# Optimization experiments

Measured on AMD Instinct MI355X. Metric: run time of the kernel, lower is better.

## Reference

```python
import jax, jax.numpy as jnp
import numpy as np
import math

B, N, DIM, H, DH, NNULL = 2, 2048, 1024, 16, 64, 2
SCALE = 8.0
LN_EPS = 1e-5


def _alibi_slopes(heads):
    # heads is a power of 2 here (16): slopes = start * start**i
    start = 2.0 ** (-(2.0 ** (-(math.log2(heads) - 3))))
    return np.array([start * (start ** i) for i in range(heads)], dtype=np.float32)


def setup_inputs() -> dict:
    key = jax.random.key(0)
    ks = jax.random.split(key, 6)
    inner = H * DH
    return {
        "x": jax.random.normal(ks[0], (B, N, DIM), dtype=jnp.float32),
        "norm_g": jnp.ones((DIM,), jnp.float32),
        "norm_b": jnp.zeros((DIM,), jnp.float32),
        "Wq": jax.random.normal(ks[1], (DIM, inner), jnp.float32) * 0.02,
        "Wkv": jax.random.normal(ks[2], (DIM, 2 * inner), jnp.float32) * 0.02,
        "q_scale": jnp.ones((DH,), jnp.float32),
        "k_scale": jnp.ones((DH,), jnp.float32),
        "null_kv": jax.random.normal(ks[3], (H, 2 * NNULL, DH), jnp.float32),
        "Wout": jax.random.normal(ks[4], (inner, DIM), jnp.float32) * 0.02,
    }


def _l2norm(t):
    # matches F.normalize: x / max(||x||, 1e-12)
    n = jnp.sqrt(jnp.sum(t * t, axis=-1, keepdims=True))
    return t / jnp.maximum(n, 1e-12)


def reference(x, norm_g, norm_b, Wq, Wkv, q_scale, k_scale, null_kv, Wout):
    b, n, dim = x.shape
    h, dh, nn = H, DH, NNULL
    j = n + nn

    # NOTE: faithful to source -- K/V come from the PRE-norm x (kv_input bound
    # before x = self.norm(x)); only Q uses the LayerNorm'd x.
    mu = jnp.mean(x, axis=-1, keepdims=True)
    var = jnp.mean((x - mu) ** 2, axis=-1, keepdims=True)
    xn = (x - mu) * jax.lax.rsqrt(var + LN_EPS) * norm_g + norm_b

    q = (xn @ Wq).reshape(b, n, h, dh).transpose(0, 2, 1, 3)          # b h n d
    kv = x @ Wkv
    k, v = jnp.split(kv, 2, axis=-1)
    k = k.reshape(b, n, h, dh).transpose(0, 2, 1, 3)                   # b h n d
    v = v.reshape(b, n, h, dh).transpose(0, 2, 1, 3)

    # null kv: (h, 2*nn, dh) -> (h, nn, 2, dh)
    null = null_kv.reshape(h, nn, 2, dh)
    nk = jnp.broadcast_to(null[:, :, 0, :][None], (b, h, nn, dh))
    nv = jnp.broadcast_to(null[:, :, 1, :][None], (b, h, nn, dh))
    k = jnp.concatenate([nk, k], axis=2)                               # b h j d
    v = jnp.concatenate([nv, v], axis=2)

    q = _l2norm(q) * q_scale
    k = _l2norm(k) * k_scale

    sim = jnp.einsum('bhid,bhjd->bhij', q, k) * SCALE                  # b h n j

    # ALiBi bias: rows at positions j-n..j-1, cols 0..j-1
    irow = jnp.arange(j - n, j)
    jcol = jnp.arange(j)
    bias = -jnp.abs(jcol[None, :] - irow[:, None]).astype(sim.dtype)   # (n, j)
    slopes = jnp.asarray(_alibi_slopes(h))[:, None, None]              # (h,1,1)
    sim = sim + slopes * bias

    # causal mask: triu with offset j - n + 1 (null kv always visible)
    causal = jnp.triu(jnp.ones((n, j), dtype=bool), k=j - n + 1)
    neg = jnp.finfo(sim.dtype).max
    sim = jnp.where(causal[None, None], -neg, sim)

    attn = jax.nn.softmax(sim, axis=-1)
    out = jnp.einsum('bhij,bhjd->bhid', attn, v)
    out = out.transpose(0, 2, 1, 3).reshape(b, n, h * dh)
    return out @ Wout
```

## Files before the change

### kernel.cpp

```cpp
#include <hip/hip_runtime.h>
#include <hip/hip_bf16.h>
#include <stdint.h>

#define H_    16
#define N_    2048
#define DIM_  1024
#define DH_   64
#define NN_   2
#define J_    2050
#define JP_   2112
#define B_    2
#define M_    4096
#define NSEG_ 84

typedef unsigned short u16;
typedef unsigned int u32;
typedef short bf16x8 __attribute__((ext_vector_type(8)));
typedef float f32x4 __attribute__((ext_vector_type(4)));

__device__ __forceinline__ u16 f2b(float f) {
  union { float f; unsigned int i; } v; v.f = f;
  unsigned int r = v.i + 0x7fffu + ((v.i >> 16) & 1u);
  return (u16)(r >> 16);
}
__device__ __forceinline__ float b2f(u16 u) {
  union { unsigned int i; float f; } v; v.i = ((unsigned int)u) << 16; return v.f;
}
__device__ __forceinline__ float lo2f(u32 u) {
  union { u32 i; float f; } v; v.i = u << 16; return v.f;
}
__device__ __forceinline__ float hi2f(u32 u) {
  union { u32 i; float f; } v; v.i = u & 0xffff0000u; return v.f;
}
__device__ __forceinline__ void unp8(const uint4 u, float* d) {
  d[0] = lo2f(u.x); d[1] = hi2f(u.x); d[2] = lo2f(u.y); d[3] = hi2f(u.y);
  d[4] = lo2f(u.z); d[5] = hi2f(u.z); d[6] = lo2f(u.w); d[7] = hi2f(u.w);
}
__device__ __forceinline__ u32 pk2(float a, float b) {
  union { __hip_bfloat162 h; u32 u; } x;
  x.h = __float22bfloat162_rn(make_float2(a, b));
  return x.u;
}
__device__ __forceinline__ void dma16(const u16* g, u16* l) {
  __builtin_amdgcn_global_load_lds(
      (const __attribute__((address_space(1))) u32*)(const void*)g,
      (__attribute__((address_space(3))) u32*)(void*)l, 16, 0, 0);
}

__global__ __launch_bounds__(256) void wtrans_k(const float* __restrict__ Wq,
                                                const float* __restrict__ Wkv,
                                                const float* __restrict__ Wout,
                                                u16* __restrict__ WqT,
                                                u16* __restrict__ WkvT,
                                                u16* __restrict__ WoutT) {
  __shared__ float tile[32][33];
  int bx = blockIdx.x;
  const float* in; u16* out; int C, cx;
  if (bx < 32)      { in = Wq;   out = WqT;   C = 1024; cx = bx; }
  else if (bx < 96) { in = Wkv;  out = WkvT;  C = 2048; cx = bx - 32; }
  else              { in = Wout; out = WoutT; C = 1024; cx = bx - 96; }
  const int R = 1024;
  int tx = threadIdx.x & 31, ty = threadIdx.x >> 5;
  int c0 = cx * 32, r0 = blockIdx.y * 32;
  #pragma unroll
  for (int i = 0; i < 32; i += 8)
    tile[ty + i][tx] = in[(size_t)(r0 + ty + i) * C + c0 + tx];
  __syncthreads();
  #pragma unroll
  for (int i = 0; i < 32; i += 8)
    out[(size_t)(c0 + ty + i) * R + r0 + tx] = f2b(tile[tx][ty + i]);
}

__global__ __launch_bounds__(256) void lnorm_k(const float* __restrict__ x,
                                               const float* __restrict__ g,
                                               const float* __restrict__ bb,
                                               u16* __restrict__ xn,
                                               u16* __restrict__ xbf) {
  int row = blockIdx.x;
  int t = threadIdx.x;
  float4 rw = *(const float4*)(x + (size_t)row * DIM_ + t * 4);
  float v0 = rw.x, v1 = rw.y, v2 = rw.z, v3 = rw.w;
  uint2 cw;
  cw.x = pk2(v0, v1);
  cw.y = pk2(v2, v3);
  *(uint2*)(xbf + (size_t)row * DIM_ + t * 4) = cw;
  float s = v0 + v1 + v2 + v3;
  float ss = v0 * v0 + v1 * v1 + v2 * v2 + v3 * v3;
  #pragma unroll
  for (int o = 32; o; o >>= 1) { s += __shfl_xor(s, o, 64); ss += __shfl_xor(ss, o, 64); }
  __shared__ float red[8];
  int lane = t & 63, w = t >> 6;
  if (lane == 0) { red[w] = s; red[4 + w] = ss; }
  __syncthreads();
  float S = red[0] + red[1] + red[2] + red[3];
  float SS = red[4] + red[5] + red[6] + red[7];
  float mu = S * (1.0f / DIM_);
  float var = SS * (1.0f / DIM_) - mu * mu;
  float rs = rsqrtf(var + 1e-5f);
  float4 gv = *(const float4*)(g + t * 4);
  float4 bv = *(const float4*)(bb + t * 4);
  uint2 ow;
  ow.x = pk2((v0 - mu) * rs * gv.x + bv.x, (v1 - mu) * rs * gv.y + bv.y);
  ow.y = pk2((v2 - mu) * rs * gv.z + bv.z, (v3 - mu) * rs * gv.w + bv.w);
  *(uint2*)(xn + (size_t)row * DIM_ + t * 4) = ow;
}

__device__ __forceinline__ void gemm_core(const u16* __restrict__ A,
                                          const u16* __restrict__ BT,
                                          int row0, int col0, int wv, int lane,
                                          u16* __restrict__ Bs, f32x4 acc[2][4]) {
  int fm = lane & 15, fg = lane >> 4;
  int srow = lane >> 3;
  int skb = ((lane & 7) ^ srow) * 8;
  const u16* Bg = BT + (size_t)(col0 + wv * 16 + srow) * 1024 + skb;
  u16* BsW = Bs + (wv * 16) * 64;
  const u16* Ag = A + (size_t)(row0 + wv * 32 + fm) * 1024 + fg * 8;
  int fr7 = fm & 7;
  int ak0 = (fg ^ fr7) * 8;
  int ak1 = ((fg + 4) ^ fr7) * 8;
  bf16x8 a0[2], a1[2];
  a0[0] = *(const bf16x8*)(Ag);
  a0[1] = *(const bf16x8*)(Ag + 16 * 1024);
  a1[0] = *(const bf16x8*)(Ag + 32);
  a1[1] = *(const bf16x8*)(Ag + 16 * 1024 + 32);
  for (int k0 = 0; k0 < 1024; k0 += 64) {
    __syncthreads();
    dma16(Bg + k0,                   BsW);
    dma16(Bg + (size_t)8 * 1024 + k0, BsW + 8 * 64);
    __syncthreads();
    bf16x8 b0[4], b1[4];
    #pragma unroll
    for (int nt = 0; nt < 4; nt++) {
      int rbase = (nt * 16 + fm) * 64;
      b0[nt] = *(const bf16x8*)&Bs[rbase + ak0];
      b1[nt] = *(const bf16x8*)&Bs[rbase + ak1];
    }
    int kn = (k0 + 64 < 1024) ? k0 + 64 : 960;
    bf16x8 na0[2], na1[2];
    {
      const u16* An = Ag + kn;
      na0[0] = *(const bf16x8*)(An);
      na0[1] = *(const bf16x8*)(An + 16 * 1024);
      na1[0] = *(const bf16x8*)(An + 32);
      na1[1] = *(const bf16x8*)(An + 16 * 1024 + 32);
    }
    #pragma unroll
    for (int mt = 0; mt < 2; mt++)
      #pragma unroll
      for (int nt = 0; nt < 4; nt++) {
        acc[mt][nt] = __builtin_amdgcn_mfma_f32_16x16x32_bf16(a0[mt], b0[nt], acc[mt][nt], 0, 0, 0);
        acc[mt][nt] = __builtin_amdgcn_mfma_f32_16x16x32_bf16(a1[mt], b1[nt], acc[mt][nt], 0, 0, 0);
      }
    a0[0] = na0[0]; a0[1] = na0[1]; a1[0] = na1[0]; a1[1] = na1[1];
  }
}

__global__ __launch_bounds__(256) void gemm_qkv(const u16* __restrict__ xn,
                                                const u16* __restrict__ xbf,
                                                const u16* __restrict__ WqT,
                                                const u16* __restrict__ WkvT,
                                                u16* __restrict__ Qn,
                                                u16* __restrict__ Kb,
                                                u16* __restrict__ Vb,
                                                const float* __restrict__ qs,
                                                const float* __restrict__ ks) {
  __shared__ u16 Bs[64 * 64];
  int tid = threadIdx.x, wv = tid >> 6, lane = tid & 63;
  int fm = lane & 15, fg = lane >> 4;
  int bx = blockIdx.x, row0 = blockIdx.y * 128;
  bool qpath = bx < 16;
  const u16* A  = qpath ? xn : xbf;
  const u16* BT = qpath ? WqT : WkvT;
  int col0 = qpath ? bx * 64 : (bx - 16) * 64;
  f32x4 acc[2][4] = {};
  gemm_core(A, BT, row0, col0, wv, lane, Bs, acc);
  bool isK = qpath || (col0 < 1024);
  int h = (qpath ? col0 : (isK ? col0 : col0 - 1024)) >> 6;
  const float* sc = qpath ? qs : ks;
  float sv[4];
  if (isK) {
    #pragma unroll
    for (int nt = 0; nt < 4; nt++) sv[nt] = sc[nt * 16 + fm];
  }
  u16* Do = qpath ? Qn : (isK ? Kb : Vb);
  #pragma unroll
  for (int mt = 0; mt < 2; mt++) {
    #pragma unroll
    for (int r = 0; r < 4; r++) {
      float inv = 1.0f;
      if (isK) {
        float ssp = 0.0f;
        #pragma unroll
        for (int nt = 0; nt < 4; nt++) ssp += acc[mt][nt][r] * acc[mt][nt][r];
        #pragma unroll
        for (int o = 1; o <= 8; o <<= 1) ssp += __shfl_xor(ssp, o, 64);
        inv = 1.0f / fmaxf(sqrtf(ssp), 1e-12f);
      }
      int m = row0 + wv * 32 + mt * 16 + fg * 4 + r;
      int b = m >> 11, n = m & 2047;
      size_t base;
      if (qpath)     base = (((size_t)(b * H_ + h)) * N_ + n) * 64;
      else if (isK)  base = (((size_t)(b * H_ + h)) * JP_ + (n + NN_)) * 64;
      else           base = (((size_t)(b * H_ + h)) * J_ + (n + NN_)) * 64;
      #pragma unroll
      for (int nt = 0; nt < 4; nt++) {
        float val = acc[mt][nt][r];
        if (isK) val = val * inv * sv[nt];
        Do[base + nt * 16 + fm] = f2b(val);
      }
    }
  }
}

__global__ __launch_bounds__(256) void gemm_out(const u16* __restrict__ AO,
                                                const u16* __restrict__ WoutT,
                                                float* __restrict__ out) {
  __shared__ u16 Bs[64 * 64];
  int tid = threadIdx.x, wv = tid >> 6, lane = tid & 63;
  int fm = lane & 15, fg = lane >> 4;
  int row0 = blockIdx.y * 128, col0 = blockIdx.x * 64;
  f32x4 acc[2][4] = {};
  gemm_core(AO, WoutT, row0, col0, wv, lane, Bs, acc);
  #pragma unroll
  for (int mt = 0; mt < 2; mt++)
    #pragma unroll
    for (int r = 0; r < 4; r++) {
      int m = row0 + wv * 32 + mt * 16 + fg * 4 + r;
      #pragma unroll
      for (int nt = 0; nt < 4; nt++)
        out[(size_t)m * 1024 + col0 + nt * 16 + fm] = acc[mt][nt][r];
    }
}

__global__ __launch_bounds__(256) void vtransp_k(const u16* __restrict__ Vb,
                                                 const float* __restrict__ nkv,
                                                 const float* __restrict__ ks,
                                                 u16* __restrict__ Kb,
                                                 u16* __restrict__ VTp) {
  __shared__ u16 tile[64][80];
  int t = threadIdx.x;
  int c = blockIdx.x, bh = blockIdx.y, h = bh & 15;
  int jl = t >> 2, dc = (t & 3) * 16;
  int j = c * 64 + jl;
  if (j < NN_) {
    float kvv[16];
    float kssp = 0.0f;
    #pragma unroll
    for (int e = 0; e < 16; e++) {
      float vv = nkv[(size_t)(h * 4 + 2 * j + 1) * 64 + dc + e];
      tile[jl][dc + e] = f2b(vv);
      float kv = nkv[(size_t)(h * 4 + 2 * j) * 64 + dc + e];
      kvv[e] = kv; kssp += kv * kv;
    }
    kssp += __shfl_xor(kssp, 1, 64);
    kssp += __shfl_xor(kssp, 2, 64);
    float inv = 1.0f / fmaxf(sqrtf(kssp), 1e-12f);
    #pragma unroll
    for (int e = 0; e < 16; e++)
      Kb[((size_t)bh * JP_ + j) * 64 + dc + e] = f2b(kvv[e] * inv * ks[dc + e]);
  } else if (j < J_) {
    const uint4* src = (const uint4*)(Vb + ((size_t)bh * J_ + j) * 64 + dc);
    *(uint4*)&tile[jl][dc] = src[0];
    *(uint4*)&tile[jl][dc + 8] = src[1];
  } else {
    uint4 z = {0, 0, 0, 0};
    *(uint4*)&tile[jl][dc] = z;
    *(uint4*)&tile[jl][dc + 8] = z;
    uint4* kz = (uint4*)(Kb + ((size_t)bh * JP_ + j) * 64 + dc);
    kz[0] = z; kz[1] = z;
  }
  __syncthreads();
  int d = t >> 2, p0 = (t & 3) * 16;
  u16 tmp[16] __attribute__((aligned(16)));
  #pragma unroll
  for (int e = 0; e < 16; e++) {
    int pos = p0 + e;
    int h2 = pos >> 5, rem = pos & 31;
    int fgp = rem >> 3, tt = rem & 7;
    int nt = tt >> 2, r = tt & 3;
    int jloc = (h2 * 2 + nt) * 16 + fgp * 4 + r;
    tmp[e] = tile[jloc][d];
  }
  uint4* dstp = (uint4*)(VTp + ((size_t)bh * 64 + d) * JP_ + c * 64 + p0);
  dstp[0] = ((uint4*)tmp)[0];
  dstp[1] = ((uint4*)tmp)[1];
}

__global__ __launch_bounds__(256, 6) void attn_k(const u16* __restrict__ Qn,
                                                 const u16* __restrict__ Kb,
                                                 const u16* __restrict__ VTp,
                                                 const float* __restrict__ qs,
                                                 const float* __restrict__ ks,
                                                 u16* __restrict__ partials) {
  __shared__ u16 Ks0[64 * 32], Ks1[64 * 32];
  __shared__ u16 Vs0[64 * 32], Vs1[64 * 32];
  int tid = threadIdx.x;
  int wv = tid >> 6, lane = tid & 63;
  int fm = lane & 15, fg = lane >> 4;
  int bh = blockIdx.y, h = bh & 15;
  int cum = 0, qt = 0, seg = 0;
  #pragma unroll 1
  for (int i = 0; i < 32; i++) {
    int t = 31 - i, s = (t + 9) >> 3;
    if ((int)blockIdx.x < cum + s) { qt = t; seg = (int)blockIdx.x - cum; break; }
    cum += s;
  }
  int q0 = qt * 64;
  int q = q0 + wv * 16 + fm;
  float slope = exp2f(-0.5f * (float)(h + 1));
  float prod = fabsf(qs[lane] * ks[lane]);
  #pragma unroll
  for (int o = 32; o; o >>= 1) prod = fmaxf(prod, __shfl_xor(prod, o, 64));
  float Mb = 8.0f * prod;
  const u16* qp = Qn + ((size_t)bh * N_ + q) * 64 + fg * 8;
  bf16x8 qf0 = *(const bf16x8*)(qp);
  bf16x8 qf1 = *(const bf16x8*)(qp + 32);
  f32x4 accO[4] = {};
  float lp = 0.0f;
  int lr = lane >> 2;
  int kbs = ((lane & 3) ^ ((lane >> 3) & 3)) * 8;
  int fs = (fg ^ ((fm >> 1) & 3)) * 8;
  const u16* KbBH = Kb + (size_t)bh * JP_ * 64;
  const u16* VTbh = VTp + (size_t)bh * 64 * JP_;
  int c0 = seg * 8;
  int c1 = min(c0 + 8, qt + 2);
  for (int c = c0; c < c1; c++) {
    int jb = c * 64;
    __syncthreads();
    const u16* Kg = KbBH + (size_t)(jb + wv * 16 + lr) * 64 + kbs;
    dma16(Kg,      Ks0 + wv * 512);
    dma16(Kg + 32, Ks1 + wv * 512);
    const u16* Vg = VTbh + (size_t)(wv * 16 + lr) * JP_ + jb + kbs;
    dma16(Vg,      Vs0 + wv * 512);
    dma16(Vg + 32, Vs1 + wv * 512);
    __syncthreads();
    f32x4 accS[4] = {};
    #pragma unroll
    for (int nt = 0; nt < 4; nt++) {
      bf16x8 kf0 = *(const bf16x8*)&Ks0[(nt * 16 + fm) * 32 + fs];
      accS[nt] = __builtin_amdgcn_mfma_f32_16x16x32_bf16(kf0, qf0, accS[nt], 0, 0, 0);
      bf16x8 kf1 = *(const bf16x8*)&Ks1[(nt * 16 + fm) * 32 + fs];
      accS[nt] = __builtin_amdgcn_mfma_f32_16x16x32_bf16(kf1, qf1, accS[nt], 0, 0, 0);
    }
    union { bf16x8 v; u16 s[8]; } P0, P1;
    #pragma unroll
    for (int nt = 0; nt < 4; nt++) {
      #pragma unroll
      for (int r = 0; r < 4; r++) {
        int jj = jb + nt * 16 + fg * 4 + r;
        float arg = fmaf(accS[nt][r], 8.0f, slope * (float)(jj - q - 2)) - Mb;
        float p = (jj <= q + 2) ? __expf(arg) : 0.0f;
        u16 pb = f2b(p);
        lp += b2f(pb);
        if (nt < 2) P0.s[nt * 4 + r] = pb;
        else        P1.s[(nt - 2) * 4 + r] = pb;
      }
    }
    #pragma unroll
    for (int nt = 0; nt < 4; nt++) {
      bf16x8 vf0 = *(const bf16x8*)&Vs0[(nt * 16 + fm) * 32 + fs];
      accO[nt] = __builtin_amdgcn_mfma_f32_16x16x32_bf16(vf0, P0.v, accO[nt], 0, 0, 0);
      bf16x8 vf1 = *(const bf16x8*)&Vs1[(nt * 16 + fm) * 32 + fs];
      accO[nt] = __builtin_amdgcn_mfma_f32_16x16x32_bf16(vf1, P1.v, accO[nt], 0, 0, 0);
    }
  }
  lp += __shfl_xor(lp, 16, 64);
  lp += __shfl_xor(lp, 32, 64);
  u16* P = partials + ((size_t)bh * NSEG_ + blockIdx.x) * 4224;
  int sq = wv * 16 + fm;
  #pragma unroll
  for (int nt = 0; nt < 4; nt++) {
    uint2 ow;
    ow.x = pk2(accO[nt][0], accO[nt][1]);
    ow.y = pk2(accO[nt][2], accO[nt][3]);
    *(uint2*)(P + sq * 64 + nt * 16 + fg * 4) = ow;
  }
  if (fg == 0) *(float*)(P + 4096 + 2 * sq) = lp;
}

__global__ __launch_bounds__(256) void comb_k(const u16* __restrict__ partials,
                                              u16* __restrict__ AO) {
  int qt = blockIdx.x, bh = blockIdx.y, b = bh >> 4, h = bh & 15;
  int t = threadIdx.x, q = t >> 2, dq = (t & 3) * 16;
  int s = (qt + 9) >> 3;
  int cum = 0;
  for (int tt = qt + 1; tt < 32; tt++) cum += (tt + 9) >> 3;
  float acc[16] = {};
  float lsum = 0.0f;
  for (int k = 0; k < s; k++) {
    const u16* P = partials + ((size_t)bh * NSEG_ + cum + k) * 4224;
    uint4 a = *(const uint4*)(P + q * 64 + dq);
    uint4 bq = *(const uint4*)(P + q * 64 + dq + 8);
    float tmp[8];
    unp8(a, tmp);
    #pragma unroll
    for (int e = 0; e < 8; e++) acc[e] += tmp[e];
    unp8(bq, tmp);
    #pragma unroll
    for (int e = 0; e < 8; e++) acc[8 + e] += tmp[e];
    lsum += *(const float*)(P + 4096 + 2 * q);
  }
  float linv = 1.0f / lsum;
  int n = qt * 64 + q;
  u16* dst = AO + (((size_t)(b * N_ + n)) * H_ + h) * 64 + dq;
  u16 ov[16] __attribute__((aligned(16)));
  #pragma unroll
  for (int e = 0; e < 16; e++) ov[e] = f2b(acc[e] * linv);
  *(uint4*)dst = ((uint4*)ov)[0];
  *(uint4*)(dst + 8) = ((uint4*)ov)[1];
}

extern "C" void kernel_launch(void* const* d_in, const int* in_sizes, int n_in,
                              void* d_out, int out_size, void* d_ws, size_t ws_size,
                              hipStream_t stream) {
  const float* x    = (const float*)d_in[0];
  const float* ng   = (const float*)d_in[1];
  const float* nb   = (const float*)d_in[2];
  const float* Wq   = (const float*)d_in[3];
  const float* Wkv  = (const float*)d_in[4];
  const float* qs   = (const float*)d_in[5];
  const float* ks   = (const float*)d_in[6];
  const float* nkv  = (const float*)d_in[7];
  const float* Wout = (const float*)d_in[8];
  float* out = (float*)d_out;
  char* ws = (char*)d_ws;

  u16* xn    = (u16*)(ws + 0);
  u16* WoutT = (u16*)(ws + 8388608);
  u16* Qn    = (u16*)(ws + 10485760);
  u16* Kb    = (u16*)(ws + 18874368);
  u16* VTp   = (u16*)(ws + 27525120);
  u16* xbf   = (u16*)(ws + 36175872);
  u16* WqT   = (u16*)(ws + 44564480);
  u16* WkvT  = (u16*)(ws + 46661632);
  u16* Vb    = (u16*)(ws + 50855936);
  u16* parts = xbf;
  u16* AO    = xn;

  wtrans_k<<<dim3(128, 32), 256, 0, stream>>>(Wq, Wkv, Wout, WqT, WkvT, WoutT);
  lnorm_k<<<4096, 256, 0, stream>>>(x, ng, nb, xn, xbf);
  gemm_qkv<<<dim3(48, 32), 256, 0, stream>>>(xn, xbf, WqT, WkvT, Qn, Kb, Vb, qs, ks);
  vtransp_k<<<dim3(33, 32), 256, 0, stream>>>(Vb, nkv, ks, Kb, VTp);
  attn_k<<<dim3(NSEG_, 32), 256, 0, stream>>>(Qn, Kb, VTp, qs, ks, parts);
  comb_k<<<dim3(32, 32), 256, 0, stream>>>(parts, AO);
  gemm_out<<<dim3(16, 32), 256, 0, stream>>>(AO, WoutT, out);
}
```

Measured before the change: 240.9 us.

## Merge layernorm and weight transpose kernels; stage 256-wide K tiles in GEMMs

The layernorm and weight-transpose/bf16-cast kernels are merged into one launch, with blocks split by index: 4096 layernorm rows and 4096 transpose tiles. The shared GEMM core now stages a 64x256 B tile in LDS per barrier pair instead of 64x64, using an XOR swizzle over 32 chunks. This cuts the number of __syncthreads and DMA rounds in the K loop by a factor of four. The cost is 32KB of LDS per block, which may limit occupancy, and a fixed min-blocks launch bound of 4.

```diff
diff --git a/kernel.cpp b/kernel.cpp
--- a/kernel.cpp
+++ b/kernel.cpp
@@ -47,62 +47,65 @@
       (__attribute__((address_space(3))) u32*)(void*)l, 16, 0, 0);
 }
 
-__global__ __launch_bounds__(256) void wtrans_k(const float* __restrict__ Wq,
-                                                const float* __restrict__ Wkv,
-                                                const float* __restrict__ Wout,
-                                                u16* __restrict__ WqT,
-                                                u16* __restrict__ WkvT,
-                                                u16* __restrict__ WoutT) {
+__global__ __launch_bounds__(256) void prep_k(const float* __restrict__ x,
+                                              const float* __restrict__ g,
+                                              const float* __restrict__ bb,
+                                              u16* __restrict__ xn,
+                                              u16* __restrict__ xbf,
+                                              const float* __restrict__ Wq,
+                                              const float* __restrict__ Wkv,
+                                              const float* __restrict__ Wout,
+                                              u16* __restrict__ WqT,
+                                              u16* __restrict__ WkvT,
+                                              u16* __restrict__ WoutT) {
   __shared__ float tile[32][33];
+  __shared__ float red[8];
   int bx = blockIdx.x;
-  const float* in; u16* out; int C, cx;
-  if (bx < 32)      { in = Wq;   out = WqT;   C = 1024; cx = bx; }
-  else if (bx < 96) { in = Wkv;  out = WkvT;  C = 2048; cx = bx - 32; }
-  else              { in = Wout; out = WoutT; C = 1024; cx = bx - 96; }
-  const int R = 1024;
-  int tx = threadIdx.x & 31, ty = threadIdx.x >> 5;
-  int c0 = cx * 32, r0 = blockIdx.y * 32;
-  #pragma unroll
-  for (int i = 0; i < 32; i += 8)
-    tile[ty + i][tx] = in[(size_t)(r0 + ty + i) * C + c0 + tx];
-  __syncthreads();
-  #pragma unroll
-  for (int i = 0; i < 32; i += 8)
-    out[(size_t)(c0 + ty + i) * R + r0 + tx] = f2b(tile[tx][ty + i]);
-}
-
-__global__ __launch_bounds__(256) void lnorm_k(const float* __restrict__ x,
-                                               const float* __restrict__ g,
-                                               const float* __restrict__ bb,
-                                               u16* __restrict__ xn,
-                                               u16* __restrict__ xbf) {
-  int row = blockIdx.x;
-  int t = threadIdx.x;
-  float4 rw = *(const float4*)(x + (size_t)row * DIM_ + t * 4);
-  float v0 = rw.x, v1 = rw.y, v2 = rw.z, v3 = rw.w;
-  uint2 cw;
-  cw.x = pk2(v0, v1);
-  cw.y = pk2(v2, v3);
-  *(uint2*)(xbf + (size_t)row * DIM_ + t * 4) = cw;
-  float s = v0 + v1 + v2 + v3;
-  float ss = v0 * v0 + v1 * v1 + v2 * v2 + v3 * v3;
-  #pragma unroll
-  for (int o = 32; o; o >>= 1) { s += __shfl_xor(s, o, 64); ss += __shfl_xor(ss, o, 64); }
-  __shared__ float red[8];
-  int lane = t & 63, w = t >> 6;
-  if (lane == 0) { red[w] = s; red[4 + w] = ss; }
-  __syncthreads();
-  float S = red[0] + red[1] + red[2] + red[3];
-  float SS = red[4] + red[5] + red[6] + red[7];
-  float mu = S * (1.0f / DIM_);
-  float var = SS * (1.0f / DIM_) - mu * mu;
-  float rs = rsqrtf(var + 1e-5f);
-  float4 gv = *(const float4*)(g + t * 4);
-  float4 bv = *(const float4*)(bb + t * 4);
-  uint2 ow;
-  ow.x = pk2((v0 - mu) * rs * gv.x + bv.x, (v1 - mu) * rs * gv.y + bv.y);
-  ow.y = pk2((v2 - mu) * rs * gv.z + bv.z, (v3 - mu) * rs * gv.w + bv.w);
-  *(uint2*)(xn + (size_t)row * DIM_ + t * 4) = ow;
+  if (bx < 4096) {
+    int row = bx;
+    int t = threadIdx.x;
+    float4 rw = *(const float4*)(x + (size_t)row * DIM_ + t * 4);
+    float v0 = rw.x, v1 = rw.y, v2 = rw.z, v3 = rw.w;
+    uint2 cw;
+    cw.x = pk2(v0, v1);
+    cw.y = pk2(v2, v3);
+    *(uint2*)(xbf + (size_t)row * DIM_ + t * 4) = cw;
+    float s = v0 + v1 + v2 + v3;
+    float ss = v0 * v0 + v1 * v1 + v2 * v2 + v3 * v3;
+    #pragma unroll
+    for (int o = 32; o; o >>= 1) { s += __shfl_xor(s, o, 64); ss += __shfl_xor(ss, o, 64); }
+    int lane = t & 63, w = t >> 6;
+    if (lane == 0) { red[w] = s; red[4 + w] = ss; }
+    __syncthreads();
+    float S = red[0] + red[1] + red[2] + red[3];
+    float SS = red[4] + red[5] + red[6] + red[7];
+    float mu = S * (1.0f / DIM_);
+    float var = SS * (1.0f / DIM_) - mu * mu;
+    float rs = rsqrtf(var + 1e-5f);
+    float4 gv = *(const float4*)(g + t * 4);
+    float4 bv = *(const float4*)(bb + t * 4);
+    uint2 ow;
+    ow.x = pk2((v0 - mu) * rs * gv.x + bv.x, (v1 - mu) * rs * gv.y + bv.y);
+    ow.y = pk2((v2 - mu) * rs * gv.z + bv.z, (v3 - mu) * rs * gv.w + bv.w);
+    *(uint2*)(xn + (size_t)row * DIM_ + t * 4) = ow;
+  } else {
+    int i = bx - 4096;
+    int cxr = i & 127, ry = i >> 7;
+    const float* in; u16* out; int C, cx;
+    if (cxr < 32)      { in = Wq;   out = WqT;   C = 1024; cx = cxr; }
+    else if (cxr < 96) { in = Wkv;  out = WkvT;  C = 2048; cx = cxr - 32; }
+    else               { in = Wout; out = WoutT; C = 1024; cx = cxr - 96; }
+    const int R = 1024;
+    int tx = threadIdx.x & 31, ty = threadIdx.x >> 5;
+    int c0 = cx * 32, r0 = ry * 32;
+    #pragma unroll
+    for (int k = 0; k < 32; k += 8)
+      tile[ty + k][tx] = in[(size_t)(r0 + ty + k) * C + c0 + tx];
+    __syncthreads();
+    #pragma unroll
+    for (int k = 0; k < 32; k += 8)
+      out[(size_t)(c0 + ty + k) * R + r0 + tx] = f2b(tile[tx][ty + k]);
+  }
 }
 
 __device__ __forceinline__ void gemm_core(const u16* __restrict__ A,
@@ -110,61 +113,63 @@
                                           int row0, int col0, int wv, int lane,
                                           u16* __restrict__ Bs, f32x4 acc[2][4]) {
   int fm = lane & 15, fg = lane >> 4;
-  int srow = lane >> 3;
-  int skb = ((lane & 7) ^ srow) * 8;
-  const u16* Bg = BT + (size_t)(col0 + wv * 16 + srow) * 1024 + skb;
-  u16* BsW = Bs + (wv * 16) * 64;
+  int l5 = lane & 31, lh = lane >> 5;
   const u16* Ag = A + (size_t)(row0 + wv * 32 + fm) * 1024 + fg * 8;
-  int fr7 = fm & 7;
-  int ak0 = (fg ^ fr7) * 8;
-  int ak1 = ((fg + 4) ^ fr7) * 8;
-  bf16x8 a0[2], a1[2];
-  a0[0] = *(const bf16x8*)(Ag);
-  a0[1] = *(const bf16x8*)(Ag + 16 * 1024);
-  a1[0] = *(const bf16x8*)(Ag + 32);
-  a1[1] = *(const bf16x8*)(Ag + 16 * 1024 + 32);
-  for (int k0 = 0; k0 < 1024; k0 += 64) {
-    __syncthreads();
-    dma16(Bg + k0,                   BsW);
-    dma16(Bg + (size_t)8 * 1024 + k0, BsW + 8 * 64);
-    __syncthreads();
-    bf16x8 b0[4], b1[4];
-    #pragma unroll
-    for (int nt = 0; nt < 4; nt++) {
-      int rbase = (nt * 16 + fm) * 64;
-      b0[nt] = *(const bf16x8*)&Bs[rbase + ak0];
-      b1[nt] = *(const bf16x8*)&Bs[rbase + ak1];
-    }
-    int kn = (k0 + 64 < 1024) ? k0 + 64 : 960;
-    bf16x8 na0[2], na1[2];
-    {
+  bf16x8 aC[4], aN[4];
+  aC[0] = *(const bf16x8*)(Ag);
+  aC[1] = *(const bf16x8*)(Ag + 16 * 1024);
+  aC[2] = *(const bf16x8*)(Ag + 32);
+  aC[3] = *(const bf16x8*)(Ag + 16 * 1024 + 32);
+  for (int ko = 0; ko < 1024; ko += 256) {
+    __syncthreads();
+    #pragma unroll
+    for (int d = 0; d < 8; d++) {
+      int rg = wv * 16 + d * 2 + lh;
+      int kb = l5 ^ (rg & 31);
+      dma16(BT + (size_t)(col0 + rg) * 1024 + ko + kb * 8,
+            Bs + (size_t)(wv * 16 + d * 2) * 256);
+    }
+    __syncthreads();
+    #pragma unroll
+    for (int ks = 0; ks < 256; ks += 64) {
+      int kn = (ks == 192) ? ko + 256 : ko + ks + 64;
+      if (kn >= 1024) kn = 0;
       const u16* An = Ag + kn;
-      na0[0] = *(const bf16x8*)(An);
-      na0[1] = *(const bf16x8*)(An + 16 * 1024);
-      na1[0] = *(const bf16x8*)(An + 32);
-      na1[1] = *(const bf16x8*)(An + 16 * 1024 + 32);
-    }
-    #pragma unroll
-    for (int mt = 0; mt < 2; mt++)
+      aN[0] = *(const bf16x8*)(An);
+      aN[1] = *(const bf16x8*)(An + 16 * 1024);
+      aN[2] = *(const bf16x8*)(An + 32);
+      aN[3] = *(const bf16x8*)(An + 16 * 1024 + 32);
+      bf16x8 b0[4], b1[4];
       #pragma unroll
       for (int nt = 0; nt < 4; nt++) {
-        acc[mt][nt] = __builtin_amdgcn_mfma_f32_16x16x32_bf16(a0[mt], b0[nt], acc[mt][nt], 0, 0, 0);
-        acc[mt][nt] = __builtin_amdgcn_mfma_f32_16x16x32_bf16(a1[mt], b1[nt], acc[mt][nt], 0, 0, 0);
+        int row = nt * 16 + fm;
+        int base = row * 256;
+        int r5 = row & 31;
+        b0[nt] = *(const bf16x8*)&Bs[base + (((ks >> 3) + fg) ^ r5) * 8];
+        b1[nt] = *(const bf16x8*)&Bs[base + (((ks >> 3) + 4 + fg) ^ r5) * 8];
       }
-    a0[0] = na0[0]; a0[1] = na0[1]; a1[0] = na1[0]; a1[1] = na1[1];
-  }
-}
-
-__global__ __launch_bounds__(256) void gemm_qkv(const u16* __restrict__ xn,
-                                                const u16* __restrict__ xbf,
-                                                const u16* __restrict__ WqT,
-                                                const u16* __restrict__ WkvT,
-                                                u16* __restrict__ Qn,
-                                                u16* __restrict__ Kb,
-                                                u16* __restrict__ Vb,
-                                                const float* __restrict__ qs,
-                                                const float* __restrict__ ks) {
-  __shared__ u16 Bs[64 * 64];
+      #pragma unroll
+      for (int mt = 0; mt < 2; mt++)
+        #pragma unroll
+        for (int nt = 0; nt < 4; nt++) {
+          acc[mt][nt] = __builtin_amdgcn_mfma_f32_16x16x32_bf16(aC[mt], b0[nt], acc[mt][nt], 0, 0, 0);
+          acc[mt][nt] = __builtin_amdgcn_mfma_f32_16x16x32_bf16(aC[2 + mt], b1[nt], acc[mt][nt], 0, 0, 0);
+        }
+      aC[0] = aN[0]; aC[1] = aN[1]; aC[2] = aN[2]; aC[3] = aN[3];
+    }
+  }
+}
+
+__global__ __launch_bounds__(256, 4) void gemm_qkv(const u16* __restrict__ xn,
+                                                   const u16* __restrict__ xbf,
+                                                   const u16* __restrict__ WqT,
+                                                   const u16* __restrict__ WkvT,
+                                                   u16* __restrict__ Qn,
+                                                   u16* __restrict__ Kb,
+                                                   u16* __restrict__ Vb,
+                                                   const float* __restrict__ qs,
+                                                   const float* __restrict__ ks) {
+  __shared__ u16 Bs[64 * 256];
   int tid = threadIdx.x, wv = tid >> 6, lane = tid & 63;
   int fm = lane & 15, fg = lane >> 4;
   int bx = blockIdx.x, row0 = blockIdx.y * 128;
@@ -212,10 +217,10 @@
   }
 }
 
-__global__ __launch_bounds__(256) void gemm_out(const u16* __restrict__ AO,
-                                                const u16* __restrict__ WoutT,
-                                                float* __restrict__ out) {
-  __shared__ u16 Bs[64 * 64];
+__global__ __launch_bounds__(256, 4) void gemm_out(const u16* __restrict__ AO,
+                                                   const u16* __restrict__ WoutT,
+                                                   float* __restrict__ out) {
+  __shared__ u16 Bs[64 * 256];
   int tid = threadIdx.x, wv = tid >> 6, lane = tid & 63;
   int fm = lane & 15, fg = lane >> 4;
   int row0 = blockIdx.y * 128, col0 = blockIdx.x * 64;
@@ -437,8 +442,7 @@
   u16* parts = xbf;
   u16* AO    = xn;
 
-  wtrans_k<<<dim3(128, 32), 256, 0, stream>>>(Wq, Wkv, Wout, WqT, WkvT, WoutT);
-  lnorm_k<<<4096, 256, 0, stream>>>(x, ng, nb, xn, xbf);
+  prep_k<<<8192, 256, 0, stream>>>(x, ng, nb, xn, xbf, Wq, Wkv, Wout, WqT, WkvT, WoutT);
   gemm_qkv<<<dim3(48, 32), 256, 0, stream>>>(xn, xbf, WqT, WkvT, Qn, Kb, Vb, qs, ks);
   vtransp_k<<<dim3(33, 32), 256, 0, stream>>>(Vb, nkv, ks, Kb, VTp);
   attn_k<<<dim3(NSEG_, 32), 256, 0, stream>>>(Qn, Kb, VTp, qs, ks, parts);
```

Result: slower. 252.0 us (+4.6%).
